# Kernel tuning notes

Hardware: AMD Instinct MI355X
Metric: run time of the kernel (lower is better)

The kernel has to match this reference:

```python
import jax, jax.numpy as jnp
import numpy as np

K, STRIDE, PAD = 3, 1, 1


def _unfold(x, k=K, stride=STRIDE, pad=PAD):
    # x: [B, C, H, W] -> patches [B, C*k*k, L] (im2col, torch nn.Unfold layout:
    # channel index = c*k*k + ki*k + kj)
    p = jax.lax.conv_general_dilated_patches(
        x, filter_shape=(k, k), window_strides=(stride, stride),
        padding=((pad, pad), (pad, pad)))  # [B, C*k*k, Ho, Wo]
    B = x.shape[0]
    return p.reshape(B, p.shape[1], -1)


def reference(x, weight, dweight, bias):
    B, C, H, W = x.shape
    O = weight.shape[0]
    cols = _unfold(x)                                   # [B, C*k*k, L]
    # scalar gate per spatial position: dweight . sigmoid(cols)
    gate = jnp.einsum('f,bfl->bl', dweight.reshape(-1), jax.nn.sigmoid(cols))
    gated = cols * gate[:, None, :]                     # [B, C*k*k, L]
    out = jnp.einsum('of,bfl->bol', weight.reshape(O, -1), gated)  # [B, O, L]
    out = out + bias[None, :, None]
    Ho, Wo = (H // 2, W // 2) if STRIDE == 2 else (H, W)
    return out.reshape(B, O, Ho, Wo)


def setup_inputs() -> dict:
    key = jax.random.key(0)
    k1, k2, k3, k4 = jax.random.split(key, 4)
    B, C, O, H, W = 8, 32, 32, 256, 256
    fan_out = O * K * K
    std = float(np.sqrt(2.0 / fan_out))
    return {
        'x': jax.random.normal(k1, (B, C, H, W), dtype=jnp.float32),
        'weight': jax.random.normal(k2, (O, C, K, K), dtype=jnp.float32) * std,
        'dweight': jax.random.normal(k3, (1, C, K, K), dtype=jnp.float32) * std,
        'bias': jax.random.normal(k4, (O,), dtype=jnp.float32),
    }
```

## Files before the change

### kernel.cpp

```cpp
#include <hip/hip_runtime.h>


typedef _Float16 half8 __attribute__((ext_vector_type(8)));
typedef _Float16 half2 __attribute__((ext_vector_type(2)));
typedef float f32x16 __attribute__((ext_vector_type(16)));

#define BATCH 8
#define CIN 32
#define COUT 32
#define TW 32
#define TH 8
#define HTW 34
#define HTH 10
#define CSTR 40
#define NCHUNK 18
#define NLDSA 14
#define NREGA (NCHUNK - NLDSA)
#define NPOS (HTH*HTW)
#define NT 4

__global__ __launch_bounds__(256) void prep_pack(const float* __restrict__ w,
                                                 const float* __restrict__ dw,
                                                 _Float16* __restrict__ Apack,
                                                 half2* __restrict__ dwf2) {
  int t = blockIdx.x * 256 + threadIdx.x;
  if (t < 9216) {
    int q = t >> 9, lane = (t >> 3) & 63, j = t & 7;
    int tap = q >> 1, h = q & 1;
    int o = lane & 31, lh = lane >> 5;
    int c = h * 16 + lh * 8 + j;
    Apack[t] = (_Float16)w[o * 288 + c * 9 + tap];
  } else if (t < 9216 + 144) {
    int i = t - 9216;
    int cp = i / 9, tap = i - cp * 9;
    half2 d;
    d.x = (_Float16)dw[(2 * cp) * 9 + tap];
    d.y = (_Float16)dw[(2 * cp + 1) * 9 + tap];
    dwf2[i] = d;
  }
}

__global__ __launch_bounds__(512, 2) void dynconv(
    const float* __restrict__ x, const _Float16* __restrict__ Apack,
    const half2* __restrict__ dwf2, const float* __restrict__ bias,
    float* __restrict__ out) {
  __shared__ __align__(16) _Float16 lvA[NLDSA * 512];
  __shared__ __align__(16) _Float16 lv[2][NPOS * CSTR];
  __shared__ _Float16 gpart[2][9 * NPOS];

  const int bid0 = blockIdx.x;
  const int bb = bid0 & 7, idx = bid0 >> 3;
  const int xh = idx & 1, yt = idx >> 1;
  const int x0b = xh * (NT * TW), y0 = yt * TH;
  const int tid = threadIdx.x;
  const int lane = tid & 63;

  half8 areg[NREGA];
#pragma unroll
  for (int r = 0; r < NREGA; ++r)
    areg[r] = *(const half8*)(Apack + (((NLDSA + r) * 64 + lane) << 3));

  half8 acopy0 = *(const half8*)(Apack + (tid << 3));
  half8 acopy1;
  if (tid < NLDSA * 64 - 512)
    acopy1 = *(const half8*)(Apack + ((512 + tid) << 3));

  const bool owner = tid < NPOS;
  const int yy = tid / HTW, xx = tid - (tid / HTW) * HTW;
  const int gy = y0 + yy - 1;
  const bool rowok = (unsigned)gy < 256u;

  float v[CIN];
  if (owner) {
    const int gx = x0b + xx - 1;
    if (rowok && (unsigned)gx < 256u) {
#pragma unroll
      for (int c = 0; c < CIN; ++c)
        v[c] = x[(((size_t)(bb * CIN + c)) << 16) + (gy << 8) + gx];
    } else {
#pragma unroll
      for (int c = 0; c < CIN; ++c) v[c] = 0.f;
    }
  }

  *(half8*)(lvA + (tid << 3)) = acopy0;
  if (tid < NLDSA * 64 - 512)
    *(half8*)(lvA + ((512 + tid) << 3)) = acopy1;

  const int w8 = tid >> 6;
  const int ln = lane & 31, lh = lane >> 5;

#pragma unroll
  for (int t = 0; t < NT; ++t) {
    const int buf = t & 1;

    float p[9];
    _Float16 hv[CIN];
    if (owner) {
#pragma unroll
      for (int tap = 0; tap < 9; ++tap) p[tap] = 0.f;
#pragma unroll
      for (int cp = 0; cp < CIN / 2; ++cp) {
        const float v0 = v[2 * cp], v1 = v[2 * cp + 1];
        const float s0 = __builtin_amdgcn_rcpf(1.f + __expf(-v0));
        const float s1 = __builtin_amdgcn_rcpf(1.f + __expf(-v1));
        half2 s2;
        s2.x = (_Float16)s0;
        s2.y = (_Float16)s1;
        hv[2 * cp] = (_Float16)v0;
        hv[2 * cp + 1] = (_Float16)v1;
#pragma unroll
        for (int tap = 0; tap < 9; ++tap) {
          const half2 d2 = dwf2[cp * 9 + tap];
#if __has_builtin(__builtin_amdgcn_fdot2)
          p[tap] = __builtin_amdgcn_fdot2(s2, d2, p[tap], false);
#else
          p[tap] += (float)s2.x * (float)d2.x + (float)s2.y * (float)d2.y;
#endif
        }
      }
      if (t + 1 < NT) {
        const int gx = x0b + (t + 1) * TW + xx - 1;
        if (rowok && (unsigned)gx < 256u) {
#pragma unroll
          for (int c = 0; c < CIN; ++c)
            v[c] = x[(((size_t)(bb * CIN + c)) << 16) + (gy << 8) + gx];
        } else {
#pragma unroll
          for (int c = 0; c < CIN; ++c) v[c] = 0.f;
        }
      }
#pragma unroll
      for (int u = 0; u < 4; ++u)
        *(half8*)(&lv[buf][tid * CSTR + u * 8]) = *(const half8*)(hv + u * 8);
#pragma unroll
      for (int tap = 0; tap < 9; ++tap)
        gpart[buf][tap * NPOS + tid] = (_Float16)p[tap];
    }

    asm volatile("s_waitcnt lgkmcnt(0)" ::: "memory");
    __builtin_amdgcn_s_barrier();
    asm volatile("" ::: "memory");

    float gate = 0.f;
#pragma unroll
    for (int ki = 0; ki < 3; ++ki)
#pragma unroll
      for (int kj = 0; kj < 3; ++kj)
        gate += (float)gpart[buf][(ki * 3 + kj) * NPOS + (w8 + ki) * HTW + ln + kj];

    f32x16 acc;
#pragma unroll
    for (int i = 0; i < 16; ++i) acc[i] = 0.f;

#pragma unroll
    for (int q = 0; q < NCHUNK; ++q) {
      const int tap = q >> 1, h = q & 1;
      const int ki = tap / 3, kj = tap - ki * 3;
      const half8 a = (q < NLDSA)
                          ? *(const half8*)(lvA + ((q * 64 + lane) << 3))
                          : areg[q - NLDSA];
      const int off = ((w8 + ki) * HTW + ln + kj) * CSTR + h * 16 + lh * 8;
      const half8 bv = *(const half8*)(&lv[buf][off]);
      acc = __builtin_amdgcn_mfma_f32_32x32x16_f16(a, bv, acc, 0, 0, 0);
    }

    const int voff_out = ((y0 + w8) << 8) + x0b + t * TW + ln;
#pragma unroll
    for (int reg = 0; reg < 16; ++reg) {
      const int o = (reg & 3) + 8 * (reg >> 2) + 4 * lh;
      out[(((size_t)(bb * COUT + o)) << 16) + voff_out] = acc[reg] * gate + bias[o];
    }
  }
}

extern "C" void kernel_launch(void* const* d_in, const int* in_sizes, int n_in,
                              void* d_out, int out_size, void* d_ws, size_t ws_size,
                              hipStream_t stream) {
  const float* x    = (const float*)d_in[0];
  const float* wgt  = (const float*)d_in[1];
  const float* dw   = (const float*)d_in[2];
  const float* bias = (const float*)d_in[3];
  float* out = (float*)d_out;

  _Float16* Apack = (_Float16*)d_ws;
  half2* dwf2     = (half2*)((char*)d_ws + 18432);

  prep_pack<<<(9216 + 144 + 255) / 256, 256, 0, stream>>>(wgt, dw, Apack, dwf2);
  dynconv<<<BATCH * 32 * 2, 512, 0, stream>>>(x, Apack, dwf2, bias, out);
}
```

Measured before the change: 138.3 us.

## Warp-specialize conv kernel into producer and MFMA consumer waves

Splits each block into 6 producer waves and 4 consumer waves. Producer waves load x, compute the sigmoid gate partials and stage fp16 tiles into LDS. Consumer waves run the MFMA contraction one tile behind, two rows each, so tile preparation and matrix math overlap across the double-buffered LDS stages. The register prefetch of the next x tile is dropped. The block grows to 640 threads with launch bounds asking for 5 blocks per CU, which caps registers per thread tightly and risks spills. LDS use per block still limits how many blocks can actually be resident.

```diff
diff --git a/kernel.cpp b/kernel.cpp
--- a/kernel.cpp
+++ b/kernel.cpp
@@ -18,6 +18,9 @@
 #define NREGA (NCHUNK - NLDSA)
 #define NPOS (HTH*HTW)
 #define NT 4
+#define NPW 6
+#define NCW 4
+#define NTHR ((NPW+NCW)*64)
 
 __global__ __launch_bounds__(256) void prep_pack(const float* __restrict__ w,
                                                  const float* __restrict__ dw,
@@ -40,7 +43,7 @@
   }
 }
 
-__global__ __launch_bounds__(512, 2) void dynconv(
+__global__ __launch_bounds__(NTHR, 5) void dynconv(
     const float* __restrict__ x, const _Float16* __restrict__ Apack,
     const half2* __restrict__ dwf2, const float* __restrict__ bias,
     float* __restrict__ out) {
@@ -54,51 +57,49 @@
   const int x0b = xh * (NT * TW), y0 = yt * TH;
   const int tid = threadIdx.x;
   const int lane = tid & 63;
-
-  half8 areg[NREGA];
-#pragma unroll
-  for (int r = 0; r < NREGA; ++r)
-    areg[r] = *(const half8*)(Apack + (((NLDSA + r) * 64 + lane) << 3));
+  const int w8 = tid >> 6;
+  const bool isP = w8 < NPW;
 
   half8 acopy0 = *(const half8*)(Apack + (tid << 3));
   half8 acopy1;
-  if (tid < NLDSA * 64 - 512)
-    acopy1 = *(const half8*)(Apack + ((512 + tid) << 3));
+  if (tid < NLDSA * 64 - NTHR)
+    acopy1 = *(const half8*)(Apack + ((NTHR + tid) << 3));
+  *(half8*)(lvA + (tid << 3)) = acopy0;
+  if (tid < NLDSA * 64 - NTHR)
+    *(half8*)(lvA + ((NTHR + tid) << 3)) = acopy1;
 
-  const bool owner = tid < NPOS;
+  half8 areg[NREGA];
+  if (!isP) {
+#pragma unroll
+    for (int r = 0; r < NREGA; ++r)
+      areg[r] = *(const half8*)(Apack + (((NLDSA + r) * 64 + lane) << 3));
+  }
+
+  const bool owner = isP && (tid < NPOS);
   const int yy = tid / HTW, xx = tid - (tid / HTW) * HTW;
   const int gy = y0 + yy - 1;
   const bool rowok = (unsigned)gy < 256u;
 
-  float v[CIN];
-  if (owner) {
-    const int gx = x0b + xx - 1;
-    if (rowok && (unsigned)gx < 256u) {
-#pragma unroll
-      for (int c = 0; c < CIN; ++c)
-        v[c] = x[(((size_t)(bb * CIN + c)) << 16) + (gy << 8) + gx];
-    } else {
-#pragma unroll
-      for (int c = 0; c < CIN; ++c) v[c] = 0.f;
-    }
-  }
-
-  *(half8*)(lvA + (tid << 3)) = acopy0;
-  if (tid < NLDSA * 64 - 512)
-    *(half8*)(lvA + ((512 + tid) << 3)) = acopy1;
-
-  const int w8 = tid >> 6;
   const int ln = lane & 31, lh = lane >> 5;
 
+  for (int t = 0; t <= NT; ++t) {
+    if (t < NT && owner) {
+      const int buf = t & 1;
+      const int gx = x0b + t * TW + xx - 1;
+      float v[CIN];
+      if (rowok && (unsigned)gx < 256u) {
+        const int voff = (gy << 8) + gx;
 #pragma unroll
-  for (int t = 0; t < NT; ++t) {
-    const int buf = t & 1;
-
-    float p[9];
-    _Float16 hv[CIN];
-    if (owner) {
+        for (int c = 0; c < CIN; ++c)
+          v[c] = x[(((size_t)(bb * CIN + c)) << 16) + voff];
+      } else {
+#pragma unroll
+        for (int c = 0; c < CIN; ++c) v[c] = 0.f;
+      }
+      float p[9];
 #pragma unroll
       for (int tap = 0; tap < 9; ++tap) p[tap] = 0.f;
+      _Float16 hv[CIN];
 #pragma unroll
       for (int cp = 0; cp < CIN / 2; ++cp) {
         const float v0 = v[2 * cp], v1 = v[2 * cp + 1];
@@ -119,17 +120,6 @@
 #endif
         }
       }
-      if (t + 1 < NT) {
-        const int gx = x0b + (t + 1) * TW + xx - 1;
-        if (rowok && (unsigned)gx < 256u) {
-#pragma unroll
-          for (int c = 0; c < CIN; ++c)
-            v[c] = x[(((size_t)(bb * CIN + c)) << 16) + (gy << 8) + gx];
-        } else {
-#pragma unroll
-          for (int c = 0; c < CIN; ++c) v[c] = 0.f;
-        }
-      }
 #pragma unroll
       for (int u = 0; u < 4; ++u)
         *(half8*)(&lv[buf][tid * CSTR + u * 8]) = *(const half8*)(hv + u * 8);
@@ -138,39 +128,48 @@
         gpart[buf][tap * NPOS + tid] = (_Float16)p[tap];
     }
 
+    if (!isP && t > 0) {
+      const int tc = t - 1, buf = tc & 1;
+      const int x0t = x0b + tc * TW;
+#pragma unroll
+      for (int rr = 0; rr < 2; ++rr) {
+        const int row = ((w8 - NPW) << 1) | rr;
+
+        float gate = 0.f;
+#pragma unroll
+        for (int ki = 0; ki < 3; ++ki)
+#pragma unroll
+          for (int kj = 0; kj < 3; ++kj)
+            gate += (float)gpart[buf][(ki * 3 + kj) * NPOS + (row + ki) * HTW + ln + kj];
+
+        f32x16 acc;
+#pragma unroll
+        for (int i = 0; i < 16; ++i) acc[i] = 0.f;
+
+#pragma unroll
+        for (int q = 0; q < NCHUNK; ++q) {
+          const int tap = q >> 1, h = q & 1;
+          const int ki = tap / 3, kj = tap - ki * 3;
+          const half8 a = (q < NLDSA)
+                              ? *(const half8*)(lvA + ((q * 64 + lane) << 3))
+                              : areg[q - NLDSA];
+          const int off = ((row + ki) * HTW + ln + kj) * CSTR + h * 16 + lh * 8;
+          const half8 bv = *(const half8*)(&lv[buf][off]);
+          acc = __builtin_amdgcn_mfma_f32_32x32x16_f16(a, bv, acc, 0, 0, 0);
+        }
+
+        const int voff_out = ((y0 + row) << 8) + x0t + ln;
+#pragma unroll
+        for (int reg = 0; reg < 16; ++reg) {
+          const int o = (reg & 3) + 8 * (reg >> 2) + 4 * lh;
+          out[(((size_t)(bb * COUT + o)) << 16) + voff_out] = acc[reg] * gate + bias[o];
+        }
+      }
+    }
+
     asm volatile("s_waitcnt lgkmcnt(0)" ::: "memory");
     __builtin_amdgcn_s_barrier();
     asm volatile("" ::: "memory");
-
-    float gate = 0.f;
-#pragma unroll
-    for (int ki = 0; ki < 3; ++ki)
-#pragma unroll
-      for (int kj = 0; kj < 3; ++kj)
-        gate += (float)gpart[buf][(ki * 3 + kj) * NPOS + (w8 + ki) * HTW + ln + kj];
-
-    f32x16 acc;
-#pragma unroll
-    for (int i = 0; i < 16; ++i) acc[i] = 0.f;
-
-#pragma unroll
-    for (int q = 0; q < NCHUNK; ++q) {
-      const int tap = q >> 1, h = q & 1;
-      const int ki = tap / 3, kj = tap - ki * 3;
-      const half8 a = (q < NLDSA)
-                          ? *(const half8*)(lvA + ((q * 64 + lane) << 3))
-                          : areg[q - NLDSA];
-      const int off = ((w8 + ki) * HTW + ln + kj) * CSTR + h * 16 + lh * 8;
-      const half8 bv = *(const half8*)(&lv[buf][off]);
-      acc = __builtin_amdgcn_mfma_f32_32x32x16_f16(a, bv, acc, 0, 0, 0);
-    }
-
-    const int voff_out = ((y0 + w8) << 8) + x0b + t * TW + ln;
-#pragma unroll
-    for (int reg = 0; reg < 16; ++reg) {
-      const int o = (reg & 3) + 8 * (reg >> 2) + 4 * lh;
-      out[(((size_t)(bb * COUT + o)) << 16) + voff_out] = acc[reg] * gate + bias[o];
-    }
   }
 }
 
@@ -187,5 +186,5 @@
   half2* dwf2     = (half2*)((char*)d_ws + 18432);
 
   prep_pack<<<(9216 + 144 + 255) / 256, 256, 0, stream>>>(wgt, dw, Apack, dwf2);
-  dynconv<<<BATCH * 32 * 2, 512, 0, stream>>>(x, Apack, dwf2, bias, out);
+  dynconv<<<BATCH * 32 * (256 / (NT * TW)), NTHR, 0, stream>>>(x, Apack, dwf2, bias, out);
 }
```

Result: slower. 186.7 us (+35.0%).
